# Optimization experiments

Hardware: AMD Instinct MI355X
Metric: run time of the kernel (lower is better)

## Reference

```python
import jax, jax.numpy as jnp
import numpy as np

IGNORE = 255


def setup_inputs() -> dict:
    key = jax.random.key(0)
    k1, k2 = jax.random.split(key)
    B, C, H, W = 4, 19, 512, 512
    out = jax.random.normal(k1, (B, C, H, W), dtype=jnp.float32)
    gt = jax.random.randint(k2, (B, H, W), 0, C, dtype=jnp.int64)
    return {"out": out, "gt": gt}


def _lovasz_softmax_flat(probas, labels):
    # probas: [P, C] softmax probabilities, labels: [P] int
    P, C = probas.shape
    valid = labels != IGNORE  # [P]
    # per-class foreground indicator (masked by valid)
    fg = ((labels[:, None] == jnp.arange(C)[None, :]) & valid[:, None]).astype(probas.dtype)  # [P, C]
    errors = jnp.abs(fg - probas)  # [P, C], values in [0, 1]
    # push ignored pixels to the end of the descending sort (error < 0)
    errors = jnp.where(valid[:, None], errors, -1.0)
    order = jnp.argsort(-errors, axis=0)  # [P, C] descending perm per class
    errors_sorted = jnp.take_along_axis(errors, order, axis=0)
    fg_sorted = jnp.take_along_axis(fg, order, axis=0)
    valid_sorted = jnp.take_along_axis(jnp.broadcast_to(valid[:, None], (P, C)), order, axis=0)
    # zero out ignored pixels' (suffix) contribution
    errors_sorted = jnp.where(valid_sorted, errors_sorted, 0.0)
    # lovasz_grad per class (ignored suffix has fg=0 and errors=0, so it is inert)
    gts = jnp.sum(fg_sorted, axis=0)  # [C]
    csum_fg = jnp.cumsum(fg_sorted, axis=0)
    intersection = gts[None, :] - csum_fg
    union = gts[None, :] + jnp.cumsum(1.0 - fg_sorted, axis=0)
    jaccard = 1.0 - intersection / union
    grad = jnp.concatenate([jaccard[:1], jnp.diff(jaccard, axis=0)], axis=0)  # [P, C]
    loss_c = jnp.sum(errors_sorted * grad, axis=0)  # [C]
    # classes='present': average over classes that appear among valid pixels
    present = gts > 0
    n_present = jnp.maximum(jnp.sum(present.astype(probas.dtype)), 1.0)
    return jnp.sum(jnp.where(present, loss_c, 0.0)) / n_present


def reference(out, gt):
    B, C, H, W = out.shape
    probas = jax.nn.softmax(out, axis=1)  # [B, C, H, W]
    probas_flat = jnp.transpose(probas, (0, 2, 3, 1)).reshape(-1, C)  # [P, C]
    labels_flat = gt.reshape(-1)  # [P]
    return _lovasz_softmax_flat(probas_flat, labels_flat)
```

## Files before the change

### kernel.cpp

```cpp
#include <hip/hip_runtime.h>
#include <stdint.h>


#define IGNORE_LBL 255
typedef unsigned long long u64;
constexpr int C_CLS = 19;
constexpr int NB = 256;
constexpr int NBT = C_CLS * NB;
constexpr int HW_C = 512 * 512;
constexpr int HIST_GRID = 512;
constexpr int HIST_NT = 1024;
constexpr int RED_Q = 8;
constexpr float ESCALE = 262144.f;

__device__ __forceinline__ int err_bin(float e) {
    unsigned u = __float_as_uint(e);
    if (u >= 0x3F800000u) return NB - 1;
    if (u < 0x3C000000u) return 0;
    int m = (int)(u >> 23) - 119;
    return (1 << m) - 1 + (int)((u & 0x7FFFFFu) >> (23 - m));
}

__global__ __launch_bounds__(HIST_NT)
void lovasz_hist_kernel(const float* __restrict__ logits,
                        const int* __restrict__ gt,
                        u64* __restrict__ part) {
    __shared__ u64 h[NBT];
    for (int i = threadIdx.x; i < NBT; i += HIST_NT) h[i] = 0ull;
    __syncthreads();

    const int gid = blockIdx.x * HIST_NT + threadIdx.x;
    const int p0 = gid * 2;
    const int b = p0 >> 18;
    const int hw = p0 & (HW_C - 1);
    const float2* base =
        (const float2*)(logits + (size_t)b * C_CLS * HW_C + hw);

    float2 v[C_CLS];
    float mx0 = -3.4e38f, mx1 = -3.4e38f;
#pragma unroll
    for (int c = 0; c < C_CLS; ++c) {
        v[c] = base[(size_t)c * (HW_C / 2)];
        mx0 = fmaxf(mx0, v[c].x);
        mx1 = fmaxf(mx1, v[c].y);
    }
    float s0 = 0.f, s1 = 0.f;
#pragma unroll
    for (int c = 0; c < C_CLS; ++c) {
        v[c].x = __expf(v[c].x - mx0);
        v[c].y = __expf(v[c].y - mx1);
        s0 += v[c].x;
        s1 += v[c].y;
    }
    const float inv0 = 1.0f / s0;
    const float inv1 = 1.0f / s1;

    const int2 lbl2 = *(const int2*)(gt + p0);
    const bool val0 = (lbl2.x != IGNORE_LBL);
    const bool val1 = (lbl2.y != IGNORE_LBL);

#pragma unroll
    for (int c = 0; c < C_CLS; ++c) {
        if (val0) {
            float prob = v[c].x * inv0;
            bool fg = (c == lbl2.x);
            float e = fmaxf(fg ? (1.0f - prob) : prob, 0.0f);
            unsigned eq = __float2uint_rn(e * ESCALE);
            u64 add = (u64)eq | (1ull << 32) | (fg ? (1ull << 46) : 0ull);
            atomicAdd(&h[c * NB + err_bin(e)], add);
        }
        if (val1) {
            float prob = v[c].y * inv1;
            bool fg = (c == lbl2.y);
            float e = fmaxf(fg ? (1.0f - prob) : prob, 0.0f);
            unsigned eq = __float2uint_rn(e * ESCALE);
            u64 add = (u64)eq | (1ull << 32) | (fg ? (1ull << 46) : 0ull);
            atomicAdd(&h[c * NB + err_bin(e)], add);
        }
    }
    __syncthreads();

    const size_t base_out = (size_t)blockIdx.x * NBT;
    for (int i = threadIdx.x; i < NBT; i += HIST_NT) part[base_out + i] = h[i];
}

__global__ __launch_bounds__(256)
void lovasz_reduce_kernel(const u64* __restrict__ part,
                          u64* __restrict__ red_es,
                          u64* __restrict__ red_cf,
                          unsigned* __restrict__ acc) {
    if (blockIdx.x == 0 && threadIdx.x < 4) acc[threadIdx.x] = 0u;
    const int q = blockIdx.x / C_CLS;
    const int seg = blockIdx.x % C_CLS;
    const int bin = seg * NB + threadIdx.x;
    const int p0 = q * (HIST_GRID / RED_Q);
    u64 es = 0; unsigned cn = 0, fgc = 0;
#pragma unroll 4
    for (int p = p0; p < p0 + HIST_GRID / RED_Q; ++p) {
        u64 x = part[(size_t)p * NBT + bin];
        es += x & 0xFFFFFFFFull;
        cn += (unsigned)((x >> 32) & 0x3FFFu);
        fgc += (unsigned)(x >> 46);
    }
    red_es[(size_t)q * NBT + bin] = es;
    red_cf[(size_t)q * NBT + bin] = (u64)cn | ((u64)fgc << 32);
}

__global__ __launch_bounds__(NB)
void lovasz_scan_kernel(const u64* __restrict__ red_es,
                        const u64* __restrict__ red_cf,
                        float* __restrict__ loss_acc,
                        int* __restrict__ pres_acc,
                        unsigned* __restrict__ done_ctr,
                        float* __restrict__ out) {
    const int c = blockIdx.x;
    const int t = threadIdx.x;
    const int lane = t & 63;
    const int wave = t >> 6;

    __shared__ u64 wtot[4];
    __shared__ u64 sh_total;

    const int db = NB - 1 - t;
    const size_t bo = (size_t)c * NB + db;
    u64 es = 0, nf = 0;
#pragma unroll
    for (int q = 0; q < RED_Q; ++q) {
        es += red_es[(size_t)q * NBT + bo];
        nf += red_cf[(size_t)q * NBT + bo];
    }
    const double mys = (double)es * (1.0 / (double)ESCALE);

    u64 incl = nf;
#pragma unroll
    for (int o = 1; o < 64; o <<= 1) {
        u64 u = __shfl_up(incl, o, 64);
        if (lane >= o) incl += u;
    }
    if (lane == 63) wtot[wave] = incl;
    __syncthreads();
    if (t == 0) {
        u64 run = 0;
#pragma unroll
        for (int w = 0; w < 4; ++w) { u64 x = wtot[w]; wtot[w] = run; run += x; }
        sh_total = run;
    }
    __syncthreads();

    const long long G = (long long)(sh_total >> 32);
    const u64 excl = wtot[wave] + (incl - nf);

    double lsum = 0.0;
    {
        long long n_b = (long long)(nf & 0xffffffffull);
        if (n_b > 0 && G > 0) {
            long long f_b = (long long)(nf >> 32);
            long long k0 = (long long)(excl & 0xffffffffull);
            long long F0 = (long long)(excl >> 32);
            long long I0 = G - F0;
            long long U0 = G + k0 - F0;
            long long F1 = F0 + f_b;
            long long I1 = G - F1;
            long long U1 = G + (k0 + n_b) - F1;
            double dJ = (double)(I0 * U1 - I1 * U0) / ((double)U0 * (double)U1);
            lsum = (mys / (double)n_b) * dJ;
        }
    }

    __shared__ double dred[4];
#pragma unroll
    for (int o = 32; o > 0; o >>= 1) lsum += __shfl_down(lsum, o, 64);
    if (lane == 0) dred[wave] = lsum;
    __syncthreads();
    if (t == 0) {
        double tot = dred[0] + dred[1] + dred[2] + dred[3];
        if (G > 0) {
            atomicAdd(loss_acc, (float)tot);
            atomicAdd(pres_acc, 1);
        }
        __threadfence();
        unsigned d = atomicAdd(done_ctr, 1u);
        if (d == C_CLS - 1) {
            float lv = atomicAdd(loss_acc, 0.0f);
            int pv = atomicAdd(pres_acc, 0);
            out[0] = lv / fmaxf((float)pv, 1.0f);
        }
    }
}

extern "C" void kernel_launch(void* const* d_in, const int* in_sizes, int n_in,
                              void* d_out, int out_size, void* d_ws, size_t ws_size,
                              hipStream_t stream) {
    const float* logits = (const float*)d_in[0];
    const int* gt = (const int*)d_in[1];
    float* out = (float*)d_out;

    size_t partBytes = (size_t)HIST_GRID * NBT * sizeof(u64);
    size_t partPad = (partBytes + 255) & ~(size_t)255;
    size_t redBytes = (size_t)RED_Q * NBT * sizeof(u64);
    size_t redPad = (redBytes + 255) & ~(size_t)255;
    u64* part = (u64*)d_ws;
    u64* red_es = (u64*)((char*)d_ws + partPad);
    u64* red_cf = (u64*)((char*)d_ws + partPad + redPad);
    unsigned* acc = (unsigned*)((char*)d_ws + partPad + 2 * redPad);
    float* loss_acc = (float*)&acc[0];
    int* pres_acc = (int*)&acc[1];
    unsigned* done_ctr = &acc[2];

    lovasz_hist_kernel<<<HIST_GRID, HIST_NT, 0, stream>>>(logits, gt, part);
    lovasz_reduce_kernel<<<RED_Q * C_CLS, 256, 0, stream>>>(part, red_es, red_cf, acc);
    lovasz_scan_kernel<<<C_CLS, NB, 0, stream>>>(red_es, red_cf,
                                                 loss_acc, pres_acc, done_ctr, out);
}
```

Measured before the change: 130.2 us.

## Process four pixels per thread and replicate shared histogram to cut atomic contention

```diff
diff --git a/kernel.cpp b/kernel.cpp
--- a/kernel.cpp
+++ b/kernel.cpp
@@ -7,9 +7,11 @@
 constexpr int C_CLS = 19;
 constexpr int NB = 256;
 constexpr int NBT = C_CLS * NB;
+constexpr int HREP = 2;
 constexpr int HW_C = 512 * 512;
-constexpr int HIST_GRID = 512;
+constexpr int HIST_GRID = 256;
 constexpr int HIST_NT = 1024;
+constexpr int PX = 4;
 constexpr int RED_Q = 8;
 constexpr float ESCALE = 262144.f;
 
@@ -25,63 +27,77 @@
 void lovasz_hist_kernel(const float* __restrict__ logits,
                         const int* __restrict__ gt,
                         u64* __restrict__ part) {
-    __shared__ u64 h[NBT];
-    for (int i = threadIdx.x; i < NBT; i += HIST_NT) h[i] = 0ull;
+    __shared__ u64 h[NBT * HREP];
+    for (int i = threadIdx.x; i < NBT * HREP; i += HIST_NT) h[i] = 0ull;
     __syncthreads();
 
     const int gid = blockIdx.x * HIST_NT + threadIdx.x;
-    const int p0 = gid * 2;
+    const int p0 = gid * PX;
     const int b = p0 >> 18;
     const int hw = p0 & (HW_C - 1);
-    const float2* base =
-        (const float2*)(logits + (size_t)b * C_CLS * HW_C + hw);
-
-    float2 v[C_CLS];
-    float mx0 = -3.4e38f, mx1 = -3.4e38f;
+    const float4* base =
+        (const float4*)(logits + (size_t)b * C_CLS * HW_C + hw);
+
+    float4 v[C_CLS];
+    float mx0 = -3.4e38f, mx1 = -3.4e38f, mx2 = -3.4e38f, mx3 = -3.4e38f;
 #pragma unroll
     for (int c = 0; c < C_CLS; ++c) {
-        v[c] = base[(size_t)c * (HW_C / 2)];
+        v[c] = base[(size_t)c * (HW_C / 4)];
         mx0 = fmaxf(mx0, v[c].x);
         mx1 = fmaxf(mx1, v[c].y);
-    }
-    float s0 = 0.f, s1 = 0.f;
+        mx2 = fmaxf(mx2, v[c].z);
+        mx3 = fmaxf(mx3, v[c].w);
+    }
+    float s0 = 0.f, s1 = 0.f, s2 = 0.f, s3 = 0.f;
 #pragma unroll
     for (int c = 0; c < C_CLS; ++c) {
         v[c].x = __expf(v[c].x - mx0);
         v[c].y = __expf(v[c].y - mx1);
+        v[c].z = __expf(v[c].z - mx2);
+        v[c].w = __expf(v[c].w - mx3);
         s0 += v[c].x;
         s1 += v[c].y;
+        s2 += v[c].z;
+        s3 += v[c].w;
     }
     const float inv0 = 1.0f / s0;
     const float inv1 = 1.0f / s1;
-
-    const int2 lbl2 = *(const int2*)(gt + p0);
-    const bool val0 = (lbl2.x != IGNORE_LBL);
-    const bool val1 = (lbl2.y != IGNORE_LBL);
+    const float inv2 = 1.0f / s2;
+    const float inv3 = 1.0f / s3;
+
+    const int4 lbl = *(const int4*)(gt + p0);
+    const bool val0 = (lbl.x != IGNORE_LBL);
+    const bool val1 = (lbl.y != IGNORE_LBL);
+    const bool val2 = (lbl.z != IGNORE_LBL);
+    const bool val3 = (lbl.w != IGNORE_LBL);
+
+    const unsigned rep = threadIdx.x & (HREP - 1);
+
+#define UPD(PV, INVV, LBV, VALV)                                              \
+    if (VALV) {                                                               \
+        float prob = (PV) * (INVV);                                           \
+        bool fg = (c == (LBV));                                               \
+        float e = fmaxf(fg ? (1.0f - prob) : prob, 0.0f);                     \
+        unsigned eq = __float2uint_rn(e * ESCALE);                            \
+        u64 add = (u64)eq | (1ull << 32) | (fg ? (1ull << 46) : 0ull);        \
+        atomicAdd(&h[((unsigned)(c * NB + err_bin(e)) << 1) | rep], add);     \
+    }
 
 #pragma unroll
     for (int c = 0; c < C_CLS; ++c) {
-        if (val0) {
-            float prob = v[c].x * inv0;
-            bool fg = (c == lbl2.x);
-            float e = fmaxf(fg ? (1.0f - prob) : prob, 0.0f);
-            unsigned eq = __float2uint_rn(e * ESCALE);
-            u64 add = (u64)eq | (1ull << 32) | (fg ? (1ull << 46) : 0ull);
-            atomicAdd(&h[c * NB + err_bin(e)], add);
-        }
-        if (val1) {
-            float prob = v[c].y * inv1;
-            bool fg = (c == lbl2.y);
-            float e = fmaxf(fg ? (1.0f - prob) : prob, 0.0f);
-            unsigned eq = __float2uint_rn(e * ESCALE);
-            u64 add = (u64)eq | (1ull << 32) | (fg ? (1ull << 46) : 0ull);
-            atomicAdd(&h[c * NB + err_bin(e)], add);
-        }
-    }
+        UPD(v[c].x, inv0, lbl.x, val0)
+        UPD(v[c].y, inv1, lbl.y, val1)
+        UPD(v[c].z, inv2, lbl.z, val2)
+        UPD(v[c].w, inv3, lbl.w, val3)
+    }
+#undef UPD
     __syncthreads();
 
     const size_t base_out = (size_t)blockIdx.x * NBT;
-    for (int i = threadIdx.x; i < NBT; i += HIST_NT) part[base_out + i] = h[i];
+    for (int i = threadIdx.x; i < NBT; i += HIST_NT) {
+        const int j = i << 1;
+        part[base_out + i] = h[j] + h[j + 1];
+    }
 }
 
 __global__ __launch_bounds__(256)
```

Result: no change. 131.8 us (+1.2%).

## Replicate shared histograms, halve bin count, skip low-error background atomics

Applied to the files above, without the earlier changes.

```diff
diff --git a/kernel.cpp b/kernel.cpp
--- a/kernel.cpp
+++ b/kernel.cpp
@@ -5,19 +5,22 @@
 #define IGNORE_LBL 255
 typedef unsigned long long u64;
 constexpr int C_CLS = 19;
-constexpr int NB = 256;
+constexpr int NB = 128;
 constexpr int NBT = C_CLS * NB;
+constexpr int HREP = 4;
 constexpr int HW_C = 512 * 512;
 constexpr int HIST_GRID = 512;
 constexpr int HIST_NT = 1024;
+constexpr int PX = 2;
 constexpr int RED_Q = 8;
 constexpr float ESCALE = 262144.f;
+constexpr float E_SKIP = 0.015625f;
 
 __device__ __forceinline__ int err_bin(float e) {
     unsigned u = __float_as_uint(e);
     if (u >= 0x3F800000u) return NB - 1;
-    if (u < 0x3C000000u) return 0;
-    int m = (int)(u >> 23) - 119;
+    if (u < 0x3D800000u) return 0;
+    int m = (int)(u >> 23) - 120;
     return (1 << m) - 1 + (int)((u & 0x7FFFFFu) >> (23 - m));
 }
 
@@ -25,12 +28,12 @@
 void lovasz_hist_kernel(const float* __restrict__ logits,
                         const int* __restrict__ gt,
                         u64* __restrict__ part) {
-    __shared__ u64 h[NBT];
-    for (int i = threadIdx.x; i < NBT; i += HIST_NT) h[i] = 0ull;
+    __shared__ u64 h[NBT * HREP];
+    for (int i = threadIdx.x; i < NBT * HREP; i += HIST_NT) h[i] = 0ull;
     __syncthreads();
 
     const int gid = blockIdx.x * HIST_NT + threadIdx.x;
-    const int p0 = gid * 2;
+    const int p0 = gid * PX;
     const int b = p0 >> 18;
     const int hw = p0 & (HW_C - 1);
     const float2* base =
@@ -59,32 +62,36 @@
     const bool val0 = (lbl2.x != IGNORE_LBL);
     const bool val1 = (lbl2.y != IGNORE_LBL);
 
+    const unsigned rep = threadIdx.x & (HREP - 1);
+
+#define UPD(PV, INVV, LBV, VALV)                                              \
+    if (VALV) {                                                               \
+        float prob = (PV) * (INVV);                                           \
+        bool fg = (c == (LBV));                                               \
+        float e = fmaxf(fg ? (1.0f - prob) : prob, 0.0f);                     \
+        if (fg || e >= E_SKIP) {                                              \
+            unsigned eq = __float2uint_rn(e * ESCALE);                        \
+            u64 add = (u64)eq | (1ull << 32) | (fg ? (1ull << 46) : 0ull);    \
+            atomicAdd(&h[((unsigned)(c * NB + err_bin(e)) << 2) | rep], add); \
+        }                                                                     \
+    }
+
 #pragma unroll
     for (int c = 0; c < C_CLS; ++c) {
-        if (val0) {
-            float prob = v[c].x * inv0;
-            bool fg = (c == lbl2.x);
-            float e = fmaxf(fg ? (1.0f - prob) : prob, 0.0f);
-            unsigned eq = __float2uint_rn(e * ESCALE);
-            u64 add = (u64)eq | (1ull << 32) | (fg ? (1ull << 46) : 0ull);
-            atomicAdd(&h[c * NB + err_bin(e)], add);
-        }
-        if (val1) {
-            float prob = v[c].y * inv1;
-            bool fg = (c == lbl2.y);
-            float e = fmaxf(fg ? (1.0f - prob) : prob, 0.0f);
-            unsigned eq = __float2uint_rn(e * ESCALE);
-            u64 add = (u64)eq | (1ull << 32) | (fg ? (1ull << 46) : 0ull);
-            atomicAdd(&h[c * NB + err_bin(e)], add);
-        }
-    }
+        UPD(v[c].x, inv0, lbl2.x, val0)
+        UPD(v[c].y, inv1, lbl2.y, val1)
+    }
+#undef UPD
     __syncthreads();
 
     const size_t base_out = (size_t)blockIdx.x * NBT;
-    for (int i = threadIdx.x; i < NBT; i += HIST_NT) part[base_out + i] = h[i];
-}
-
-__global__ __launch_bounds__(256)
+    for (int i = threadIdx.x; i < NBT; i += HIST_NT) {
+        const int j = i << 2;
+        part[base_out + i] = h[j] + h[j + 1] + h[j + 2] + h[j + 3];
+    }
+}
+
+__global__ __launch_bounds__(NB)
 void lovasz_reduce_kernel(const u64* __restrict__ part,
                           u64* __restrict__ red_es,
                           u64* __restrict__ red_cf,
@@ -118,7 +125,7 @@
     const int lane = t & 63;
     const int wave = t >> 6;
 
-    __shared__ u64 wtot[4];
+    __shared__ u64 wtot[2];
     __shared__ u64 sh_total;
 
     const int db = NB - 1 - t;
@@ -142,7 +149,7 @@
     if (t == 0) {
         u64 run = 0;
 #pragma unroll
-        for (int w = 0; w < 4; ++w) { u64 x = wtot[w]; wtot[w] = run; run += x; }
+        for (int w = 0; w < 2; ++w) { u64 x = wtot[w]; wtot[w] = run; run += x; }
         sh_total = run;
     }
     __syncthreads();
@@ -167,13 +174,13 @@
         }
     }
 
-    __shared__ double dred[4];
+    __shared__ double dred[2];
 #pragma unroll
     for (int o = 32; o > 0; o >>= 1) lsum += __shfl_down(lsum, o, 64);
     if (lane == 0) dred[wave] = lsum;
     __syncthreads();
     if (t == 0) {
-        double tot = dred[0] + dred[1] + dred[2] + dred[3];
+        double tot = dred[0] + dred[1];
         if (G > 0) {
             atomicAdd(loss_acc, (float)tot);
             atomicAdd(pres_acc, 1);
@@ -208,7 +215,7 @@
     unsigned* done_ctr = &acc[2];
 
     lovasz_hist_kernel<<<HIST_GRID, HIST_NT, 0, stream>>>(logits, gt, part);
-    lovasz_reduce_kernel<<<RED_Q * C_CLS, 256, 0, stream>>>(part, red_es, red_cf, acc);
+    lovasz_reduce_kernel<<<RED_Q * C_CLS, NB, 0, stream>>>(part, red_es, red_cf, acc);
     lovasz_scan_kernel<<<C_CLS, NB, 0, stream>>>(red_es, red_cf,
                                                  loss_acc, pres_acc, done_ctr, out);
 }
```

Measured after the change: 131.3 us. No clear change (+0.8%).
